# Optimization experiments

Measured on AMD Instinct MI355X. Metric: run time of the kernel, lower is better.

The kernel has to match this reference:

```python
import jax, jax.numpy as jnp
import numpy as np

N, E, F, H, D, B = 50000, 800000, 128, 4, 32, 8  # nodes, edges, feat, heads, head_dim, graphs
NEG_SLOPE = 0.2


def _layer_norm(x, g, b, eps=1e-5):
    mu = jnp.mean(x, axis=-1, keepdims=True)
    var = jnp.var(x, axis=-1, keepdims=True)
    return (x - mu) * jax.lax.rsqrt(var + eps) * g + b


def _gat(x, src, dst, W, a_src, a_dst, bias):
    # PyG GATConv (eval): linear -> per-node alpha terms -> edge logits ->
    # per-destination segment softmax -> scatter-add weighted messages.
    h = (x @ W).reshape(N, H, D)                                  # [N,H,D]
    al_s = jnp.einsum('nhd,hd->nh', h, a_src)                     # [N,H]
    al_d = jnp.einsum('nhd,hd->nh', h, a_dst)                     # [N,H]
    logits = jax.nn.leaky_relu(al_s[src] + al_d[dst], NEG_SLOPE)  # [E+N,H]
    m = jax.ops.segment_max(logits, dst, num_segments=N)          # [N,H]
    ex = jnp.exp(logits - m[dst])
    denom = jax.ops.segment_sum(ex, dst, num_segments=N)          # [N,H]
    alpha = ex / denom[dst]                                       # [E+N,H]
    msg = h[src] * alpha[..., None]                               # [E+N,H,D]
    out = jax.ops.segment_sum(msg, dst, num_segments=N)           # [N,H,D]
    return out.reshape(N, H * D) + bias


def _gat_block(x, src, dst, W, a_src, a_dst, bias, ln_g, ln_b):
    out = _gat(x, src, dst, W, a_src, a_dst, bias)
    return _layer_norm(out + x, ln_g, ln_b)  # residual: dims match (128==128)


def setup_inputs() -> dict:
    key = jax.random.key(0)
    ks = jax.random.split(key, 24)
    s = 0.05
    inp = {
        'x': jax.random.normal(ks[0], (N, F), jnp.float32),
        'edge_index': jax.random.randint(ks[1], (2, E), 0, N, jnp.int32),
        'batch': jnp.sort(jax.random.randint(ks[2], (N,), 0, B, jnp.int32)),
    }
    i = 3
    for p in ('loc', 'reg'):
        inp[p + '_W'] = jax.random.normal(ks[i], (F, H * D)) * s; i += 1
        inp[p + '_att_src'] = jax.random.normal(ks[i], (H, D)) * s; i += 1
        inp[p + '_att_dst'] = jax.random.normal(ks[i], (H, D)) * s; i += 1
        inp[p + '_bias'] = jnp.zeros((H * D,))
        inp[p + '_ln_g'] = jnp.ones((F,))
        inp[p + '_ln_b'] = jnp.zeros((F,))
    inp['gp_W1'] = jax.random.normal(ks[i], (F, F)) * s; i += 1
    inp['gp_b1'] = jnp.zeros((F,))
    inp['gp_W2'] = jax.random.normal(ks[i], (F, F)) * s; i += 1
    inp['gp_b2'] = jnp.zeros((F,))
    inp['fu_W1'] = jax.random.normal(ks[i], (3 * F, 2 * F)) * s; i += 1
    inp['fu_b1'] = jnp.zeros((2 * F,))
    inp['fu_W2'] = jax.random.normal(ks[i], (2 * F, F)) * s; i += 1
    inp['fu_b2'] = jnp.zeros((F,))
    inp['fu_ln_g'] = jnp.ones((F,))
    inp['fu_ln_b'] = jnp.zeros((F,))
    return inp


def reference(x, edge_index, batch,
              loc_W, loc_att_src, loc_att_dst, loc_bias, loc_ln_g, loc_ln_b,
              reg_W, reg_att_src, reg_att_dst, reg_bias, reg_ln_g, reg_ln_b,
              gp_W1, gp_b1, gp_W2, gp_b2,
              fu_W1, fu_b1, fu_W2, fu_b2, fu_ln_g, fu_ln_b):
    # add self-loops (PyG GATConv default add_self_loops=True)
    loops = jnp.arange(N, dtype=edge_index.dtype)
    src = jnp.concatenate([edge_index[0], loops])
    dst = jnp.concatenate([edge_index[1], loops])

    local = _gat_block(x, src, dst, loc_W, loc_att_src, loc_att_dst, loc_bias, loc_ln_g, loc_ln_b)
    regional = _gat_block(x, src, dst, reg_W, reg_att_src, reg_att_dst, reg_bias, reg_ln_g, reg_ln_b)

    # global mean pool per graph, broadcast back to nodes
    sums = jax.ops.segment_sum(x, batch, num_segments=B)                  # [B,F]
    cnts = jax.ops.segment_sum(jnp.ones((N, 1), x.dtype), batch, num_segments=B)
    gctx = (sums / cnts)[batch]                                           # [N,F]
    gfeat = jax.nn.relu(gctx @ gp_W1 + gp_b1) @ gp_W2 + gp_b2

    cat = jnp.concatenate([local, regional, gfeat], axis=-1)              # [N,3F]
    fused = jax.nn.relu(cat @ fu_W1 + fu_b1) @ fu_W2 + fu_b2
    return _layer_norm(fused, fu_ln_g, fu_ln_b)
```

## Files before the change

### kernel.cpp

```cpp
#include <hip/hip_runtime.h>

#define NN 50000
#define EE 800000
#define FF 128
#define HH 4
#define BB 8
#define NEG 0.2f
#define NBLK ((NN + 255) / 256)

typedef __attribute__((ext_vector_type(8))) short s8v;
typedef __attribute__((ext_vector_type(4))) float f4v;

__device__ __forceinline__ unsigned short f2b(float f) {
    union { float f; unsigned u; } v; v.f = f;
    unsigned r = v.u + 0x7fffu + ((v.u >> 16) & 1u);
    return (unsigned short)(r >> 16);
}
__device__ __forceinline__ float b2f(unsigned short h) {
    union { unsigned u; float f; } v; v.u = ((unsigned)h) << 16;
    return v.f;
}
__device__ __forceinline__ float uasf(unsigned u) {
    union { unsigned u; float f; } v; v.u = u; return v.f;
}
__device__ __forceinline__ float lrelu(float t) { return t > 0.f ? t : NEG * t; }

__global__ void k_prep(const float* __restrict__ locW, const float* __restrict__ regW,
                       const float* __restrict__ W1, const float* __restrict__ W2,
                       unsigned short* __restrict__ Wt, unsigned short* __restrict__ W1t,
                       unsigned short* __restrict__ W2t, int* cur, float* pooled) {
    int i = blockIdx.x * 256 + threadIdx.x;
    if (i < 32768) {
        int n = i >> 7, k = i & 127;
        float v = n < 128 ? locW[k * 128 + n] : regW[k * 128 + n - 128];
        Wt[i] = f2b(v);
    } else if (i < 131072) {
        int j = i - 32768; int n = j / 384, k = j - n * 384;
        W1t[j] = f2b(W1[k * 256 + n]);
    } else if (i < 163840) {
        int j = i - 131072; int n = j >> 8, k = j & 255;
        W2t[j] = f2b(W2[k * 128 + n]);
    } else {
        int j = i - 163840;
        if (j < NN) cur[j] = 1;
        if (j < BB * FF) pooled[j] = 0.f;
    }
}

__global__ void k_count(const int* __restrict__ ei, int* cur) {
    int i = blockIdx.x * 256 + threadIdx.x;
    if (i < EE) atomicAdd(&cur[ei[EE + i]], 1);
}

__global__ __launch_bounds__(256) void k_scanA(int* cur, int* row_ptr, int* bsum) {
    __shared__ int wsum[4];
    int b = blockIdx.x, t = threadIdx.x;
    int i = b * 256 + t;
    int v = (i < NN) ? cur[i] : 0;
    if (i < NN) cur[i] = 0;
    int lane = t & 63, w = t >> 6;
    int sc = v;
#pragma unroll
    for (int off = 1; off < 64; off <<= 1) {
        int n = __shfl_up(sc, off);
        if (lane >= off) sc += n;
    }
    if (lane == 63) wsum[w] = sc;
    __syncthreads();
    int woff = 0;
    for (int k = 0; k < w; k++) woff += wsum[k];
    int incl = sc + woff;
    if (i < NN) row_ptr[i + 1] = incl;
    if (t == 255) bsum[b] = incl;
    if (i == 0) row_ptr[0] = 0;
}

__global__ __launch_bounds__(256) void k_scanB(const int* __restrict__ bsum, int* boff) {
    __shared__ int wsum[4];
    int t = threadIdx.x;
    int v = (t < NBLK) ? bsum[t] : 0;
    int lane = t & 63, w = t >> 6;
    int sc = v;
#pragma unroll
    for (int off = 1; off < 64; off <<= 1) {
        int n = __shfl_up(sc, off);
        if (lane >= off) sc += n;
    }
    if (lane == 63) wsum[w] = sc;
    __syncthreads();
    int woff = 0;
    for (int k = 0; k < w; k++) woff += wsum[k];
    if (t < NBLK) boff[t] = sc + woff - v;
}

__global__ __launch_bounds__(256) void k_scanC(int* row_ptr, const int* __restrict__ boff) {
    int i = blockIdx.x * 256 + threadIdx.x;
    if (i < NN) row_ptr[i + 1] += boff[blockIdx.x];
}

__global__ void k_scatter(const int* __restrict__ ei, const int* __restrict__ row_ptr,
                          int* cur, int* col) {
    int i = blockIdx.x * 256 + threadIdx.x;
    if (i < EE) {
        int s = ei[i], d = ei[EE + i];
        int p = atomicAdd(&cur[d], 1);
        col[row_ptr[d] + p] = s;
    } else if (i < EE + NN) {
        int n = i - EE;
        int p = atomicAdd(&cur[n], 1);
        col[row_ptr[n] + p] = n;
    }
}

__global__ __launch_bounds__(256) void k_gemm1(
    const float* __restrict__ x, const int* __restrict__ batch,
    const unsigned short* __restrict__ Wt,
    const float* __restrict__ loc_as, const float* __restrict__ loc_ad,
    const float* __restrict__ reg_as, const float* __restrict__ reg_ad,
    unsigned short* __restrict__ hl, unsigned short* __restrict__ hr,
    float* __restrict__ alc_s, float* __restrict__ alc_d,
    float* __restrict__ pooled) {
    __shared__ unsigned short As[4 * 64 * 8];
    __shared__ unsigned short Bs[4 * 256 * 8];
    __shared__ unsigned short Hs[32 * 64 * 8];
    int t = threadIdx.x;
    int w = t >> 6, l = t & 63;
    int lq = l >> 4, lr = l & 15;
    int r0 = blockIdx.x * 64;

    int srow = t >> 2, sg = t & 3;
    int snode = r0 + srow; if (snode >= NN) snode = NN - 1;
    const float* xrow = x + (size_t)snode * 128 + sg * 8;

    f4v acc[4][4];
#pragma unroll
    for (int a0 = 0; a0 < 4; a0++)
#pragma unroll
        for (int b0 = 0; b0 < 4; b0++) acc[a0][b0] = (f4v){0.f, 0.f, 0.f, 0.f};

    for (int ks = 0; ks < 4; ++ks) {
        {
            float4 f0 = *(const float4*)(xrow + ks * 32);
            float4 f1 = *(const float4*)(xrow + ks * 32 + 4);
            unsigned short u[8] = { f2b(f0.x), f2b(f0.y), f2b(f0.z), f2b(f0.w),
                                    f2b(f1.x), f2b(f1.y), f2b(f1.z), f2b(f1.w) };
            *(s8v*)&As[(sg * 64 + srow) * 8] = *(const s8v*)u;
        }
#pragma unroll
        for (int it = 0; it < 4; ++it) {
            int c = t + it * 256;
            int g = c & 3, n = c >> 2;
            *(s8v*)&Bs[(g * 256 + n) * 8] = *(const s8v*)&Wt[(size_t)n * 128 + ks * 32 + g * 8];
        }
        __syncthreads();
        s8v af[4], bf[4];
#pragma unroll
        for (int rf = 0; rf < 4; ++rf) af[rf] = *(const s8v*)&As[(lq * 64 + rf * 16 + lr) * 8];
#pragma unroll
        for (int cf = 0; cf < 4; ++cf) bf[cf] = *(const s8v*)&Bs[(lq * 256 + w * 64 + cf * 16 + lr) * 8];
#pragma unroll
        for (int rf = 0; rf < 4; ++rf)
#pragma unroll
            for (int cf = 0; cf < 4; ++cf)
                acc[rf][cf] = __builtin_amdgcn_mfma_f32_16x16x32_bf16(af[rf], bf[cf], acc[rf][cf], 0, 0, 0);
        __syncthreads();
    }
#pragma unroll
    for (int cf = 0; cf < 4; ++cf) {
        int c = w * 64 + cf * 16 + lr;
#pragma unroll
        for (int rf = 0; rf < 4; ++rf)
#pragma unroll
            for (int i = 0; i < 4; ++i) {
                int row = rf * 16 + lq * 4 + i;
                Hs[((c >> 3) * 64 + row) * 8 + (c & 7)] = f2b(acc[rf][cf][i]);
            }
    }
    __syncthreads();
#pragma unroll
    for (int it = 0; it < 8; ++it) {
        int c = t + it * 256;
        int row = c >> 5, g = c & 31;
        int node = r0 + row;
        if (node < NN) {
            s8v v = *(const s8v*)&Hs[(g * 64 + row) * 8];
            int cc = g * 8;
            if (cc < 128) *(s8v*)&hl[(size_t)node * 128 + cc] = v;
            else          *(s8v*)&hr[(size_t)node * 128 + cc - 128] = v;
        }
    }
#pragma unroll
    for (int it = 0; it < 4; ++it) {
        int row = it * 16 + (t >> 4);
        int node = r0 + row;
        int q = t & 15;
        int gat = q >> 3, sd = (q >> 2) & 1, head = q & 3;
        const float* av = gat ? (sd ? reg_ad : reg_as) : (sd ? loc_ad : loc_as);
        float s = 0.f;
        int cbase = gat * 128 + head * 32;
        for (int d = 0; d < 32; ++d) {
            int c = cbase + d;
            s += b2f(Hs[((c >> 3) * 64 + row) * 8 + (c & 7)]) * av[head * 32 + d];
        }
        if (node < NN) {
            float* outp = sd ? alc_d : alc_s;
            outp[(size_t)node * 8 + gat * 4 + head] = s;
        }
    }
    {
        int colp = t & 127, halfp = t >> 7;
        int rbase = r0 + halfp * 32;
        int lastrow = r0 + 63; if (lastrow >= NN) lastrow = NN - 1;
        int blo = batch[r0 < NN ? r0 : NN - 1];
        int bhi = batch[lastrow];
        float acc0 = 0.f, acc1 = 0.f;
        for (int r = 0; r < 32; ++r) {
            int row = rbase + r;
            if (row < NN) {
                float v = x[(size_t)row * 128 + colp];
                int b = batch[row];
                if (b == blo) acc0 += v; else acc1 += v;
            }
        }
        atomicAdd(&pooled[blo * 128 + colp], acc0);
        if (bhi != blo) atomicAdd(&pooled[bhi * 128 + colp], acc1);
    }
}

__global__ __launch_bounds__(256) void k_gfeat8(
    const float* __restrict__ pooled, const int* __restrict__ batch,
    const float* __restrict__ W1, const float* __restrict__ b1,
    const float* __restrict__ W2, const float* __restrict__ b2,
    unsigned short* __restrict__ g8b) {
    __shared__ float mean_s[128];
    __shared__ float hid_s[128];
    __shared__ float part[256];
    __shared__ int bnd[2];
    int b = blockIdx.x, t = threadIdx.x;
    if (t < 2) {
        int target = b + t;
        int lo = 0, hi = NN;
        while (lo < hi) { int mid = (lo + hi) >> 1; if (batch[mid] < target) lo = mid + 1; else hi = mid; }
        bnd[t] = lo;
    }
    __syncthreads();
    int cnt = bnd[1] - bnd[0];
    float inv = cnt ? 1.f / (float)cnt : 0.f;
    if (t < 128) mean_s[t] = pooled[b * 128 + t] * inv;
    __syncthreads();
    int c = t & 127, kh = t >> 7;
    float a = 0.f;
    for (int k = kh * 64; k < kh * 64 + 64; k++) a += mean_s[k] * W1[k * 128 + c];
    part[t] = a;
    __syncthreads();
    if (t < 128) hid_s[t] = fmaxf(part[t] + part[t + 128] + b1[t], 0.f);
    __syncthreads();
    float a2 = 0.f;
    for (int k = kh * 64; k < kh * 64 + 64; k++) a2 += hid_s[k] * W2[k * 128 + c];
    part[t] = a2;
    __syncthreads();
    if (t < 128) g8b[b * 128 + t] = f2b(part[t] + part[t + 128] + b2[t]);
}

__global__ __launch_bounds__(256) void k_gat(
    const int* __restrict__ row_ptr, const int* __restrict__ col,
    const unsigned short* __restrict__ hl, const unsigned short* __restrict__ hr,
    const float* __restrict__ alc_s, const float* __restrict__ alc_d,
    const float* __restrict__ x,
    const float* __restrict__ loc_bias, const float* __restrict__ loc_g, const float* __restrict__ loc_b,
    const float* __restrict__ reg_bias, const float* __restrict__ reg_g, const float* __restrict__ reg_b,
    unsigned short* __restrict__ out_local, unsigned short* __restrict__ out_reg) {
    __shared__ float exA[4][64][4];
    __shared__ float exB[4][64][4];
    __shared__ int   colb[4][64];
    __shared__ int   degs[4];
    int w = threadIdx.x >> 6, lane = threadIdx.x & 63;
    int hA = lane >> 4;
    int node = blockIdx.x * 4 + w;
    int rp0 = row_ptr[node];
    int deg = row_ptr[node + 1] - rp0;
    if (lane == 0) degs[w] = deg;
    float4 adL = *(const float4*)&alc_d[(size_t)node * 8];
    float4 adR = *(const float4*)&alc_d[(size_t)node * 8 + 4];
    __syncthreads();
    int maxdeg = max(max(degs[0], degs[1]), max(degs[2], degs[3]));
    int chunks = (maxdeg + 63) >> 6;

    float sL0 = 0.f, sL1 = 0.f, sL2 = 0.f, sL3 = 0.f;
    float sR0 = 0.f, sR1 = 0.f, sR2 = 0.f, sR3 = 0.f;
    for (int base = 0; base < deg; base += 64) {
        int i = base + lane;
        bool v = i < deg;
        int s = col[rp0 + (v ? i : deg - 1)];
        float4 aL = *(const float4*)&alc_s[(size_t)s * 8];
        float4 aR = *(const float4*)&alc_s[(size_t)s * 8 + 4];
        float e0 = __expf(lrelu(aL.x + adL.x));
        float e1 = __expf(lrelu(aL.y + adL.y));
        float e2 = __expf(lrelu(aL.z + adL.z));
        float e3 = __expf(lrelu(aL.w + adL.w));
        float f0 = __expf(lrelu(aR.x + adR.x));
        float f1 = __expf(lrelu(aR.y + adR.y));
        float f2 = __expf(lrelu(aR.z + adR.z));
        float f3 = __expf(lrelu(aR.w + adR.w));
        if (!v) { e0 = e1 = e2 = e3 = f0 = f1 = f2 = f3 = 0.f; }
        *(float4*)&exA[w][lane][0] = make_float4(e0, e1, e2, e3);
        *(float4*)&exB[w][lane][0] = make_float4(f0, f1, f2, f3);
        colb[w][lane] = s;
        sL0 += e0; sL1 += e1; sL2 += e2; sL3 += e3;
        sR0 += f0; sR1 += f1; sR2 += f2; sR3 += f3;
    }
    __syncthreads();
#pragma unroll
    for (int off = 32; off; off >>= 1) {
        sL0 += __shfl_xor(sL0, off); sL1 += __shfl_xor(sL1, off);
        sL2 += __shfl_xor(sL2, off); sL3 += __shfl_xor(sL3, off);
        sR0 += __shfl_xor(sR0, off); sR1 += __shfl_xor(sR1, off);
        sR2 += __shfl_xor(sR2, off); sR3 += __shfl_xor(sR3, off);
    }
    float iA = (hA & 2) ? ((hA & 1) ? 1.f / sL3 : 1.f / sL2)
                        : ((hA & 1) ? 1.f / sL1 : 1.f / sL0);
    float iB = (hA & 2) ? ((hA & 1) ? 1.f / sR3 : 1.f / sR2)
                        : ((hA & 1) ? 1.f / sR1 : 1.f / sR0);

    float a0 = 0.f, a1 = 0.f, b0 = 0.f, b1 = 0.f;
    const unsigned* hlp = (const unsigned*)hl;
    const unsigned* hrp = (const unsigned*)hr;
    if (chunks == 1) {
#pragma unroll 4
        for (int e = 0; e < deg; ++e) {
            int s = colb[w][e];
            float eAv = exA[w][e][hA];
            float eBv = exB[w][e][hA];
            unsigned ul = hlp[(size_t)s * 64 + lane];
            unsigned ur = hrp[(size_t)s * 64 + lane];
            a0 += eAv * uasf(ul << 16);
            a1 += eAv * uasf(ul & 0xffff0000u);
            b0 += eBv * uasf(ur << 16);
            b1 += eBv * uasf(ur & 0xffff0000u);
        }
    } else {
        for (int c = 0; c < chunks; ++c) {
            int base = c * 64, i = base + lane;
            if (i < deg) {
                int s = col[rp0 + i];
                float4 aL = *(const float4*)&alc_s[(size_t)s * 8];
                float4 aR = *(const float4*)&alc_s[(size_t)s * 8 + 4];
                *(float4*)&exA[w][lane][0] = make_float4(
                    __expf(lrelu(aL.x + adL.x)), __expf(lrelu(aL.y + adL.y)),
                    __expf(lrelu(aL.z + adL.z)), __expf(lrelu(aL.w + adL.w)));
                *(float4*)&exB[w][lane][0] = make_float4(
                    __expf(lrelu(aR.x + adR.x)), __expf(lrelu(aR.y + adR.y)),
                    __expf(lrelu(aR.z + adR.z)), __expf(lrelu(aR.w + adR.w)));
                colb[w][lane] = s;
            }
            __syncthreads();
            int nc = deg - base; nc = nc < 0 ? 0 : (nc > 64 ? 64 : nc);
#pragma unroll 4
            for (int e = 0; e < nc; ++e) {
                int s = colb[w][e];
                float eAv = exA[w][e][hA];
                float eBv = exB[w][e][hA];
                unsigned ul = hlp[(size_t)s * 64 + lane];
                unsigned ur = hrp[(size_t)s * 64 + lane];
                a0 += eAv * uasf(ul << 16);
                a1 += eAv * uasf(ul & 0xffff0000u);
                b0 += eBv * uasf(ur << 16);
                b1 += eBv * uasf(ur & 0xffff0000u);
            }
            __syncthreads();
        }
    }

    int f = 2 * lane;
    float2 xr = *(const float2*)&x[(size_t)node * 128 + f];
    float2 lbi = *(const float2*)&loc_bias[f];
    float2 rbi = *(const float2*)&reg_bias[f];
    float v0 = a0 * iA + lbi.x + xr.x;
    float v1 = a1 * iA + lbi.y + xr.y;
    float u0 = b0 * iB + rbi.x + xr.x;
    float u1 = b1 * iB + rbi.y + xr.y;

    float sv = v0 + v1, su = u0 + u1;
#pragma unroll
    for (int off = 32; off; off >>= 1) { sv += __shfl_xor(sv, off); su += __shfl_xor(su, off); }
    float mv = sv * (1.f / 128.f), mu = su * (1.f / 128.f);
    float dv0 = v0 - mv, dv1 = v1 - mv, du0 = u0 - mu, du1 = u1 - mu;
    float qv = dv0 * dv0 + dv1 * dv1, qu = du0 * du0 + du1 * du1;
#pragma unroll
    for (int off = 32; off; off >>= 1) { qv += __shfl_xor(qv, off); qu += __shfl_xor(qu, off); }
    float rv = rsqrtf(qv * (1.f / 128.f) + 1e-5f), ru = rsqrtf(qu * (1.f / 128.f) + 1e-5f);
    float2 lg = *(const float2*)&loc_g[f], lb2 = *(const float2*)&loc_b[f];
    float2 rg = *(const float2*)&reg_g[f], rb2 = *(const float2*)&reg_b[f];
    unsigned pv = (unsigned)f2b(dv0 * rv * lg.x + lb2.x) | ((unsigned)f2b(dv1 * rv * lg.y + lb2.y) << 16);
    unsigned pu = (unsigned)f2b(du0 * ru * rg.x + rb2.x) | ((unsigned)f2b(du1 * ru * rg.y + rb2.y) << 16);
    *(unsigned*)&out_local[(size_t)node * 128 + f] = pv;
    *(unsigned*)&out_reg[(size_t)node * 128 + f]   = pu;
}

__global__ __launch_bounds__(256) void k_fusedm(
    const unsigned short* __restrict__ localb, const unsigned short* __restrict__ regionalb,
    const unsigned short* __restrict__ g8b, const int* __restrict__ batch,
    const unsigned short* __restrict__ W1t, const float* __restrict__ b1,
    const unsigned short* __restrict__ W2t, const float* __restrict__ b2,
    const float* __restrict__ lng, const float* __restrict__ lnb,
    float* __restrict__ out) {
    __shared__ unsigned short As[4 * 64 * 8];
    __shared__ unsigned short Bs[4 * 256 * 8];
    __shared__ unsigned short Hs[32 * 64 * 8];
    __shared__ unsigned short W2s[4 * 128 * 8];
    int t = threadIdx.x;
    int w = t >> 6, l = t & 63;
    int lq = l >> 4, lr = l & 15;
    int r0 = blockIdx.x * 64;

    int srow = t >> 2, sg = t & 3;
    int snode = r0 + srow; if (snode >= NN) snode = NN - 1;
    int sbatch = batch[snode];

    f4v acc[4][4];
#pragma unroll
    for (int a0 = 0; a0 < 4; a0++)
#pragma unroll
        for (int b0 = 0; b0 < 4; b0++) acc[a0][b0] = (f4v){0.f, 0.f, 0.f, 0.f};

    for (int ks = 0; ks < 12; ++ks) {
        int seg = ks >> 2;
        int ko = (ks & 3) * 32 + sg * 8;
        const unsigned short* src =
            seg == 0 ? localb + (size_t)snode * 128 + ko :
            seg == 1 ? regionalb + (size_t)snode * 128 + ko :
                       g8b + (size_t)sbatch * 128 + ko;
        *(s8v*)&As[(sg * 64 + srow) * 8] = *(const s8v*)src;
#pragma unroll
        for (int it = 0; it < 4; ++it) {
            int c = t + it * 256;
            int g = c & 3, n = c >> 2;
            *(s8v*)&Bs[(g * 256 + n) * 8] = *(const s8v*)&W1t[(size_t)n * 384 + ks * 32 + g * 8];
        }
        __syncthreads();
        s8v af[4], bf[4];
#pragma unroll
        for (int rf = 0; rf < 4; ++rf) af[rf] = *(const s8v*)&As[(lq * 64 + rf * 16 + lr) * 8];
#pragma unroll
        for (int cf = 0; cf < 4; ++cf) bf[cf] = *(const s8v*)&Bs[(lq * 256 + w * 64 + cf * 16 + lr) * 8];
#pragma unroll
        for (int rf = 0; rf < 4; ++rf)
#pragma unroll
            for (int cf = 0; cf < 4; ++cf)
                acc[rf][cf] = __builtin_amdgcn_mfma_f32_16x16x32_bf16(af[rf], bf[cf], acc[rf][cf], 0, 0, 0);
        __syncthreads();
    }
#pragma unroll
    for (int cf = 0; cf < 4; ++cf) {
        int c = w * 64 + cf * 16 + lr;
        float bc = b1[c];
#pragma unroll
        for (int rf = 0; rf < 4; ++rf)
#pragma unroll
            for (int i = 0; i < 4; ++i) {
                int row = rf * 16 + lq * 4 + i;
                float v0 = acc[rf][cf][i] + bc;
                Hs[((c >> 3) * 64 + row) * 8 + (c & 7)] = f2b(v0 > 0.f ? v0 : 0.f);
            }
    }
    __syncthreads();
    f4v a2[8];
#pragma unroll
    for (int cf = 0; cf < 8; ++cf) a2[cf] = (f4v){0.f, 0.f, 0.f, 0.f};
    for (int ks = 0; ks < 8; ++ks) {
#pragma unroll
        for (int it = 0; it < 2; ++it) {
            int c = t + it * 256;
            int g = c & 3, n = c >> 2;
            *(s8v*)&W2s[(g * 128 + n) * 8] = *(const s8v*)&W2t[(size_t)n * 256 + ks * 32 + g * 8];
        }
        __syncthreads();
        s8v af = *(const s8v*)&Hs[((ks * 4 + lq) * 64 + w * 16 + lr) * 8];
#pragma unroll
        for (int cf = 0; cf < 8; ++cf) {
            s8v bfv = *(const s8v*)&W2s[(lq * 128 + cf * 16 + lr) * 8];
            a2[cf] = __builtin_amdgcn_mfma_f32_16x16x32_bf16(af, bfv, a2[cf], 0, 0, 0);
        }
        __syncthreads();
    }
    float b2c[8], gc[8], bc2[8];
#pragma unroll
    for (int cf = 0; cf < 8; ++cf) {
        int c = cf * 16 + lr;
        b2c[cf] = b2[c]; gc[cf] = lng[c]; bc2[cf] = lnb[c];
    }
#pragma unroll
    for (int i = 0; i < 4; ++i) {
        int row = w * 16 + lq * 4 + i;
        int node = r0 + row;
        float vals[8]; float s = 0.f;
#pragma unroll
        for (int cf = 0; cf < 8; ++cf) { vals[cf] = a2[cf][i] + b2c[cf]; s += vals[cf]; }
        s += __shfl_xor(s, 1); s += __shfl_xor(s, 2); s += __shfl_xor(s, 4); s += __shfl_xor(s, 8);
        float mean = s * (1.f / 128.f);
        float vs = 0.f;
#pragma unroll
        for (int cf = 0; cf < 8; ++cf) { float d = vals[cf] - mean; vs += d * d; }
        vs += __shfl_xor(vs, 1); vs += __shfl_xor(vs, 2); vs += __shfl_xor(vs, 4); vs += __shfl_xor(vs, 8);
        float rstd = rsqrtf(vs * (1.f / 128.f) + 1e-5f);
        if (node < NN) {
#pragma unroll
            for (int cf = 0; cf < 8; ++cf)
                out[(size_t)node * 128 + cf * 16 + lr] = (vals[cf] - mean) * rstd * gc[cf] + bc2[cf];
        }
    }
}

extern "C" void kernel_launch(void* const* d_in, const int* in_sizes, int n_in,
                              void* d_out, int out_size, void* d_ws, size_t ws_size,
                              hipStream_t stream) {
    const float* x      = (const float*)d_in[0];
    const int*   ei     = (const int*)d_in[1];
    const int*   batch  = (const int*)d_in[2];
    const float* locW   = (const float*)d_in[3];
    const float* loc_as = (const float*)d_in[4];
    const float* loc_ad = (const float*)d_in[5];
    const float* loc_bi = (const float*)d_in[6];
    const float* loc_g  = (const float*)d_in[7];
    const float* loc_b  = (const float*)d_in[8];
    const float* regW   = (const float*)d_in[9];
    const float* reg_as = (const float*)d_in[10];
    const float* reg_ad = (const float*)d_in[11];
    const float* reg_bi = (const float*)d_in[12];
    const float* reg_g  = (const float*)d_in[13];
    const float* reg_b  = (const float*)d_in[14];
    const float* gp_W1  = (const float*)d_in[15];
    const float* gp_b1  = (const float*)d_in[16];
    const float* gp_W2  = (const float*)d_in[17];
    const float* gp_b2  = (const float*)d_in[18];
    const float* fu_W1  = (const float*)d_in[19];
    const float* fu_b1  = (const float*)d_in[20];
    const float* fu_W2  = (const float*)d_in[21];
    const float* fu_b2  = (const float*)d_in[22];
    const float* fu_lg  = (const float*)d_in[23];
    const float* fu_lb  = (const float*)d_in[24];
    float* out = (float*)d_out;

    char* ws = (char*)d_ws;
    size_t off = 0;
    auto alloc = [&](size_t bytes) { void* p = ws + off; off += (bytes + 255) & ~(size_t)255; return p; };
    unsigned short* hl        = (unsigned short*)alloc((size_t)NN * 128 * 2);
    unsigned short* hr        = (unsigned short*)alloc((size_t)NN * 128 * 2);
    unsigned short* localb    = (unsigned short*)alloc((size_t)NN * 128 * 2);
    unsigned short* regionalb = (unsigned short*)alloc((size_t)NN * 128 * 2);
    float* alc_s  = (float*)alloc((size_t)NN * 8 * 4);
    float* alc_d  = (float*)alloc((size_t)NN * 8 * 4);
    int* row_ptr  = (int*)alloc((size_t)(NN + 1) * 4);
    int* cur      = (int*)alloc((size_t)NN * 4);
    int* col      = (int*)alloc((size_t)(EE + NN) * 4);
    float* pooled = (float*)alloc((size_t)BB * 128 * 4);
    unsigned short* g8b = (unsigned short*)alloc((size_t)BB * 128 * 2);
    unsigned short* Wt  = (unsigned short*)alloc((size_t)32768 * 2);
    unsigned short* W1t = (unsigned short*)alloc((size_t)98304 * 2);
    unsigned short* W2t = (unsigned short*)alloc((size_t)32768 * 2);
    int* bsum = (int*)alloc((size_t)NBLK * 4);
    int* boff = (int*)alloc((size_t)NBLK * 4);

    hipLaunchKernelGGL(k_prep, dim3(640 + NBLK), dim3(256), 0, stream,
                       locW, regW, fu_W1, fu_W2, Wt, W1t, W2t, cur, pooled);
    hipLaunchKernelGGL(k_count, dim3((EE + 255) / 256), dim3(256), 0, stream, ei, cur);
    hipLaunchKernelGGL(k_scanA, dim3(NBLK), dim3(256), 0, stream, cur, row_ptr, bsum);
    hipLaunchKernelGGL(k_scanB, dim3(1), dim3(256), 0, stream, bsum, boff);
    hipLaunchKernelGGL(k_scanC, dim3(NBLK), dim3(256), 0, stream, row_ptr, boff);
    hipLaunchKernelGGL(k_scatter, dim3((EE + NN + 255) / 256), dim3(256), 0, stream, ei, row_ptr, cur, col);
    hipLaunchKernelGGL(k_gemm1, dim3((NN + 63) / 64), dim3(256), 0, stream,
                       x, batch, Wt, loc_as, loc_ad, reg_as, reg_ad,
                       hl, hr, alc_s, alc_d, pooled);
    hipLaunchKernelGGL(k_gfeat8, dim3(BB), dim3(256), 0, stream,
                       pooled, batch, gp_W1, gp_b1, gp_W2, gp_b2, g8b);
    hipLaunchKernelGGL(k_gat, dim3(NN / 4), dim3(256), 0, stream,
                       row_ptr, col, hl, hr, alc_s, alc_d, x,
                       loc_bi, loc_g, loc_b, reg_bi, reg_g, reg_b,
                       localb, regionalb);
    hipLaunchKernelGGL(k_fusedm, dim3((NN + 63) / 64), dim3(256), 0, stream,
                       localb, regionalb, g8b, batch,
                       W1t, fu_b1, W2t, fu_b2, fu_lg, fu_lb, out);
}
```

Baseline: 275.7 us.

## Double-buffer LDS tiles in GEMM kernels and merge scan passes

Adds register-prefetch double buffering to the k-loops of k_gemm1 and k_fusedm. The next K-slice is loaded from global memory while MFMAs run on the current one, which removes one barrier per iteration and hides load latency. k_fusedm reuses a single staging buffer for the W1 and W2 phases to keep LDS use in check. The separate block-offset scan kernel is removed; each k_scanC block now reduces the preceding block sums itself, saving one launch. The cost is extra registers for the prefetched fragments and more LDS in k_gemm1, which could lower occupancy.

```diff
diff --git a/kernel.cpp b/kernel.cpp
--- a/kernel.cpp
+++ b/kernel.cpp
@@ -24,6 +24,13 @@
     union { unsigned u; float f; } v; v.u = u; return v.f;
 }
 __device__ __forceinline__ float lrelu(float t) { return t > 0.f ? t : NEG * t; }
+__device__ __forceinline__ s8v cvt8(const float* p) {
+    float4 f0 = *(const float4*)p;
+    float4 f1 = *(const float4*)(p + 4);
+    unsigned short u[8] = { f2b(f0.x), f2b(f0.y), f2b(f0.z), f2b(f0.w),
+                            f2b(f1.x), f2b(f1.y), f2b(f1.z), f2b(f1.w) };
+    return *(const s8v*)u;
+}
 
 __global__ void k_prep(const float* __restrict__ locW, const float* __restrict__ regW,
                        const float* __restrict__ W1, const float* __restrict__ W2,
@@ -75,27 +82,18 @@
     if (i == 0) row_ptr[0] = 0;
 }
 
-__global__ __launch_bounds__(256) void k_scanB(const int* __restrict__ bsum, int* boff) {
-    __shared__ int wsum[4];
-    int t = threadIdx.x;
-    int v = (t < NBLK) ? bsum[t] : 0;
+__global__ __launch_bounds__(256) void k_scanC(int* row_ptr, const int* __restrict__ bsum) {
+    __shared__ int ssum[4];
+    int b = blockIdx.x, t = threadIdx.x;
     int lane = t & 63, w = t >> 6;
-    int sc = v;
-#pragma unroll
-    for (int off = 1; off < 64; off <<= 1) {
-        int n = __shfl_up(sc, off);
-        if (lane >= off) sc += n;
-    }
-    if (lane == 63) wsum[w] = sc;
-    __syncthreads();
-    int woff = 0;
-    for (int k = 0; k < w; k++) woff += wsum[k];
-    if (t < NBLK) boff[t] = sc + woff - v;
-}
-
-__global__ __launch_bounds__(256) void k_scanC(int* row_ptr, const int* __restrict__ boff) {
-    int i = blockIdx.x * 256 + threadIdx.x;
-    if (i < NN) row_ptr[i + 1] += boff[blockIdx.x];
+    int v = (t < b) ? bsum[t] : 0;
+#pragma unroll
+    for (int off = 32; off; off >>= 1) v += __shfl_xor(v, off);
+    if (lane == 0) ssum[w] = v;
+    __syncthreads();
+    int off = ssum[0] + ssum[1] + ssum[2] + ssum[3];
+    int i = b * 256 + t;
+    if (i < NN && b > 0) row_ptr[i + 1] += off;
 }
 
 __global__ void k_scatter(const int* __restrict__ ei, const int* __restrict__ row_ptr,
@@ -120,9 +118,9 @@
     unsigned short* __restrict__ hl, unsigned short* __restrict__ hr,
     float* __restrict__ alc_s, float* __restrict__ alc_d,
     float* __restrict__ pooled) {
-    __shared__ unsigned short As[4 * 64 * 8];
-    __shared__ unsigned short Bs[4 * 256 * 8];
-    __shared__ unsigned short Hs[32 * 64 * 8];
+    __shared__ __align__(16) unsigned short SA[2][2048];
+    __shared__ __align__(16) unsigned short SB[2][8192];
+    __shared__ __align__(16) unsigned short Hs[16384];
     int t = threadIdx.x;
     int w = t >> 6, l = t & 63;
     int lq = l >> 4, lr = l & 15;
@@ -138,31 +136,46 @@
 #pragma unroll
         for (int b0 = 0; b0 < 4; b0++) acc[a0][b0] = (f4v){0.f, 0.f, 0.f, 0.f};
 
+    *(s8v*)&SA[0][(sg * 64 + srow) * 8] = cvt8(xrow);
+#pragma unroll
+    for (int it = 0; it < 4; ++it) {
+        int c = t + it * 256;
+        int g = c & 3, n = c >> 2;
+        *(s8v*)&SB[0][(g * 256 + n) * 8] = *(const s8v*)&Wt[(size_t)n * 128 + g * 8];
+    }
+    __syncthreads();
+#pragma unroll
     for (int ks = 0; ks < 4; ++ks) {
-        {
-            float4 f0 = *(const float4*)(xrow + ks * 32);
-            float4 f1 = *(const float4*)(xrow + ks * 32 + 4);
-            unsigned short u[8] = { f2b(f0.x), f2b(f0.y), f2b(f0.z), f2b(f0.w),
-                                    f2b(f1.x), f2b(f1.y), f2b(f1.z), f2b(f1.w) };
-            *(s8v*)&As[(sg * 64 + srow) * 8] = *(const s8v*)u;
-        }
-#pragma unroll
-        for (int it = 0; it < 4; ++it) {
-            int c = t + it * 256;
-            int g = c & 3, n = c >> 2;
-            *(s8v*)&Bs[(g * 256 + n) * 8] = *(const s8v*)&Wt[(size_t)n * 128 + ks * 32 + g * 8];
-        }
-        __syncthreads();
+        int cur = ks & 1;
+        s8v pa; s8v pb[4];
+        if (ks < 3) {
+            pa = cvt8(xrow + (ks + 1) * 32);
+#pragma unroll
+            for (int it = 0; it < 4; ++it) {
+                int c = t + it * 256;
+                int g = c & 3, n = c >> 2;
+                pb[it] = *(const s8v*)&Wt[(size_t)n * 128 + (ks + 1) * 32 + g * 8];
+            }
+        }
         s8v af[4], bf[4];
 #pragma unroll
-        for (int rf = 0; rf < 4; ++rf) af[rf] = *(const s8v*)&As[(lq * 64 + rf * 16 + lr) * 8];
-#pragma unroll
-        for (int cf = 0; cf < 4; ++cf) bf[cf] = *(const s8v*)&Bs[(lq * 256 + w * 64 + cf * 16 + lr) * 8];
+        for (int rf = 0; rf < 4; ++rf) af[rf] = *(const s8v*)&SA[cur][(lq * 64 + rf * 16 + lr) * 8];
+#pragma unroll
+        for (int cf = 0; cf < 4; ++cf) bf[cf] = *(const s8v*)&SB[cur][(lq * 256 + w * 64 + cf * 16 + lr) * 8];
 #pragma unroll
         for (int rf = 0; rf < 4; ++rf)
 #pragma unroll
             for (int cf = 0; cf < 4; ++cf)
                 acc[rf][cf] = __builtin_amdgcn_mfma_f32_16x16x32_bf16(af[rf], bf[cf], acc[rf][cf], 0, 0, 0);
+        if (ks < 3) {
+            *(s8v*)&SA[cur ^ 1][(sg * 64 + srow) * 8] = pa;
+#pragma unroll
+            for (int it = 0; it < 4; ++it) {
+                int c = t + it * 256;
+                int g = c & 3, n = c >> 2;
+                *(s8v*)&SB[cur ^ 1][(g * 256 + n) * 8] = pb[it];
+            }
+        }
         __syncthreads();
     }
 #pragma unroll
@@ -404,10 +417,11 @@
     const unsigned short* __restrict__ W2t, const float* __restrict__ b2,
     const float* __restrict__ lng, const float* __restrict__ lnb,
     float* __restrict__ out) {
-    __shared__ unsigned short As[4 * 64 * 8];
-    __shared__ unsigned short Bs[4 * 256 * 8];
-    __shared__ unsigned short Hs[32 * 64 * 8];
-    __shared__ unsigned short W2s[4 * 128 * 8];
+    __shared__ __align__(16) unsigned short stg[20480];
+    __shared__ __align__(16) unsigned short Hs[16384];
+    unsigned short* SAb[2] = { stg, stg + 2048 };
+    unsigned short* SBb[2] = { stg + 4096, stg + 12288 };
+    unsigned short* W2Sb[2] = { stg, stg + 4096 };
     int t = threadIdx.x;
     int w = t >> 6, l = t & 63;
     int lq = l >> 4, lr = l & 15;
@@ -417,37 +431,60 @@
     int snode = r0 + srow; if (snode >= NN) snode = NN - 1;
     int sbatch = batch[snode];
 
-    f4v acc[4][4];
-#pragma unroll
-    for (int a0 = 0; a0 < 4; a0++)
-#pragma unroll
-        for (int b0 = 0; b0 < 4; b0++) acc[a0][b0] = (f4v){0.f, 0.f, 0.f, 0.f};
-
-    for (int ks = 0; ks < 12; ++ks) {
+    auto asrc = [&](int ks) -> const unsigned short* {
         int seg = ks >> 2;
         int ko = (ks & 3) * 32 + sg * 8;
-        const unsigned short* src =
-            seg == 0 ? localb + (size_t)snode * 128 + ko :
-            seg == 1 ? regionalb + (size_t)snode * 128 + ko :
-                       g8b + (size_t)sbatch * 128 + ko;
-        *(s8v*)&As[(sg * 64 + srow) * 8] = *(const s8v*)src;
-#pragma unroll
-        for (int it = 0; it < 4; ++it) {
-            int c = t + it * 256;
-            int g = c & 3, n = c >> 2;
-            *(s8v*)&Bs[(g * 256 + n) * 8] = *(const s8v*)&W1t[(size_t)n * 384 + ks * 32 + g * 8];
-        }
-        __syncthreads();
+        return seg == 0 ? localb + (size_t)snode * 128 + ko :
+               seg == 1 ? regionalb + (size_t)snode * 128 + ko :
+                          g8b + (size_t)sbatch * 128 + ko;
+    };
+
+    f4v acc[4][4];
+#pragma unroll
+    for (int a0 = 0; a0 < 4; a0++)
+#pragma unroll
+        for (int b0 = 0; b0 < 4; b0++) acc[a0][b0] = (f4v){0.f, 0.f, 0.f, 0.f};
+
+    *(s8v*)&SAb[0][(sg * 64 + srow) * 8] = *(const s8v*)asrc(0);
+#pragma unroll
+    for (int it = 0; it < 4; ++it) {
+        int c = t + it * 256;
+        int g = c & 3, n = c >> 2;
+        *(s8v*)&SBb[0][(g * 256 + n) * 8] = *(const s8v*)&W1t[(size_t)n * 384 + g * 8];
+    }
+    __syncthreads();
+#pragma unroll
+    for (int ks = 0; ks < 12; ++ks) {
+        int cur = ks & 1;
+        s8v pa; s8v pb[4];
+        if (ks < 11) {
+            pa = *(const s8v*)asrc(ks + 1);
+#pragma unroll
+            for (int it = 0; it < 4; ++it) {
+                int c = t + it * 256;
+                int g = c & 3, n = c >> 2;
+                pb[it] = *(const s8v*)&W1t[(size_t)n * 384 + (ks + 1) * 32 + g * 8];
+            }
+        }
         s8v af[4], bf[4];
 #pragma unroll
-        for (int rf = 0; rf < 4; ++rf) af[rf] = *(const s8v*)&As[(lq * 64 + rf * 16 + lr) * 8];
-#pragma unroll
-        for (int cf = 0; cf < 4; ++cf) bf[cf] = *(const s8v*)&Bs[(lq * 256 + w * 64 + cf * 16 + lr) * 8];
+        for (int rf = 0; rf < 4; ++rf) af[rf] = *(const s8v*)&SAb[cur][(lq * 64 + rf * 16 + lr) * 8];
+#pragma unroll
+        for (int cf = 0; cf < 4; ++cf) bf[cf] = *(const s8v*)&SBb[cur][(lq * 256 + w * 64 + cf * 16 + lr) * 8];
 #pragma unroll
         for (int rf = 0; rf < 4; ++rf)
 #pragma unroll
             for (int cf = 0; cf < 4; ++cf)
                 acc[rf][cf] = __builtin_amdgcn_mfma_f32_16x16x32_bf16(af[rf], bf[cf], acc[rf][cf], 0, 0, 0);
+        if (ks < 11) {
+            *(s8v*)&SAb[cur ^ 1][(sg * 64 + srow) * 8] = pa;
+#pragma unroll
+            for (int it = 0; it < 4; ++it) {
+                int c = t + it * 256;
+                int g = c & 3, n = c >> 2;
+                *(s8v*)&SBb[cur ^ 1][(g * 256 + n) * 8] = pb[it];
+            }
+        }
         __syncthreads();
     }
 #pragma unroll
@@ -464,22 +501,41 @@
             }
     }
     __syncthreads();
+#pragma unroll
+    for (int it = 0; it < 2; ++it) {
+        int c = t + it * 256;
+        int g = c & 3, n = c >> 2;
+        *(s8v*)&W2Sb[0][(g * 128 + n) * 8] = *(const s8v*)&W2t[(size_t)n * 256 + g * 8];
+    }
+    __syncthreads();
     f4v a2[8];
 #pragma unroll
     for (int cf = 0; cf < 8; ++cf) a2[cf] = (f4v){0.f, 0.f, 0.f, 0.f};
+#pragma unroll
     for (int ks = 0; ks < 8; ++ks) {
-#pragma unroll
-        for (int it = 0; it < 2; ++it) {
-            int c = t + it * 256;
-            int g = c & 3, n = c >> 2;
-            *(s8v*)&W2s[(g * 128 + n) * 8] = *(const s8v*)&W2t[(size_t)n * 256 + ks * 32 + g * 8];
-        }
-        __syncthreads();
+        int cur = ks & 1;
+        s8v pw[2];
+        if (ks < 7) {
+#pragma unroll
+            for (int it = 0; it < 2; ++it) {
+                int c = t + it * 256;
+                int g = c & 3, n = c >> 2;
+                pw[it] = *(const s8v*)&W2t[(size_t)n * 256 + (ks + 1) * 32 + g * 8];
+            }
+        }
         s8v af = *(const s8v*)&Hs[((ks * 4 + lq) * 64 + w * 16 + lr) * 8];
 #pragma unroll
         for (int cf = 0; cf < 8; ++cf) {
-            s8v bfv = *(const s8v*)&W2s[(lq * 128 + cf * 16 + lr) * 8];
+            s8v bfv = *(const s8v*)&W2Sb[cur][(lq * 128 + cf * 16 + lr) * 8];
             a2[cf] = __builtin_amdgcn_mfma_f32_16x16x32_bf16(af, bfv, a2[cf], 0, 0, 0);
+        }
+        if (ks < 7) {
+#pragma unroll
+            for (int it = 0; it < 2; ++it) {
+                int c = t + it * 256;
+                int g = c & 3, n = c >> 2;
+                *(s8v*)&W2Sb[cur ^ 1][(g * 128 + n) * 8] = pw[it];
+            }
         }
         __syncthreads();
     }
@@ -559,14 +615,12 @@
     unsigned short* W1t = (unsigned short*)alloc((size_t)98304 * 2);
     unsigned short* W2t = (unsigned short*)alloc((size_t)32768 * 2);
     int* bsum = (int*)alloc((size_t)NBLK * 4);
-    int* boff = (int*)alloc((size_t)NBLK * 4);
 
     hipLaunchKernelGGL(k_prep, dim3(640 + NBLK), dim3(256), 0, stream,
                        locW, regW, fu_W1, fu_W2, Wt, W1t, W2t, cur, pooled);
     hipLaunchKernelGGL(k_count, dim3((EE + 255) / 256), dim3(256), 0, stream, ei, cur);
     hipLaunchKernelGGL(k_scanA, dim3(NBLK), dim3(256), 0, stream, cur, row_ptr, bsum);
-    hipLaunchKernelGGL(k_scanB, dim3(1), dim3(256), 0, stream, bsum, boff);
-    hipLaunchKernelGGL(k_scanC, dim3(NBLK), dim3(256), 0, stream, row_ptr, boff);
+    hipLaunchKernelGGL(k_scanC, dim3(NBLK), dim3(256), 0, stream, row_ptr, bsum);
     hipLaunchKernelGGL(k_scatter, dim3((EE + NN + 255) / 256), dim3(256), 0, stream, ei, row_ptr, cur, col);
     hipLaunchKernelGGL(k_gemm1, dim3((NN + 63) / 64), dim3(256), 0, stream,
                        x, batch, Wt, loc_as, loc_ad, reg_as, reg_ad,
```

Result: no change. 273.1 us (-0.9%).
